# Optimization experiments

Hardware: AMD Instinct MI355X
Metric: run time of the kernel (lower is better)

The kernel has to match this reference:

```python
import jax, jax.numpy as jnp
import numpy as np

B, R, N, K, E = 128, 500, 500, 10, 128
H1 = 5 * E  # UnvisitedMLP hidden = embedding_dim * 5


def setup_inputs() -> dict:
    key = jax.random.key(0)
    ks = jax.random.split(key, 8)
    current = jax.random.randint(ks[0], (B, R), 0, N)
    distance = jax.random.uniform(ks[1], (B, N, N), dtype=jnp.float32)
    # unvisited cities, exercising the padding-index path in search_unvisited.
    visited = jax.random.uniform(ks[2], (B, R, N)) < 0.97
    masked = jnp.where(visited, -jnp.inf, 0.0).astype(jnp.float32)
    encoded_nodes = jax.random.normal(ks[3], (B, N, E), dtype=jnp.float32)
    w1 = jax.random.normal(ks[4], (H1, K * E), dtype=jnp.float32) * (1.0 / np.sqrt(K * E))
    b1 = jnp.zeros((H1,), dtype=jnp.float32)
    w2 = jax.random.normal(ks[5], (E, H1), dtype=jnp.float32) * (1.0 / np.sqrt(H1))
    b2 = jnp.zeros((E,), dtype=jnp.float32)
    return {"current": current, "distance": distance, "masked": masked,
            "encoded_nodes": encoded_nodes, "w1": w1, "b1": b1, "w2": w2, "b2": b2}


def _search_unvisited(current, distance, masked, k_near):
    # distance_filtered[b, r, :] = distance[b, current[b, r], :]  -> [B, R, N]
    b_idx = jnp.arange(current.shape[0])[:, None]
    distance_filtered = distance[b_idx, current, :]
    mask_unvisited = masked != -jnp.inf
    distance_masked = jnp.where(mask_unvisited, distance_filtered, jnp.inf)
    # k smallest == top-k of negated distances
    neg_vals, k_idx = jax.lax.top_k(-distance_masked, k_near)  # [B, R, K]
    is_inf = neg_vals == -jnp.inf  # entries that were +inf (no unvisited left)
    n_cities = distance.shape[1]
    return jnp.where(is_inf, n_cities, k_idx)  # padding index = problem_size


def _gather_pad0(encoded_nodes, idx):
    # pad encoded_nodes with a zero row at index N, then gather  -> [B, R, K, E]
    padded = jnp.concatenate(
        [encoded_nodes, jnp.zeros_like(encoded_nodes[:, :1, :])], axis=1)
    b_idx = jnp.arange(encoded_nodes.shape[0])[:, None, None]
    return padded[b_idx, idx, :]


def _pad_avg(a):
    # replace all-zero (padding) rows along K with the mean of non-zero rows
    is_zero = a.sum(axis=-1) == 0  # [B, R, K]
    nz_count = jnp.clip((~is_zero).sum(axis=-1).astype(jnp.float32), 1e-9)
    mean_vec = a.sum(axis=2) / nz_count[..., None]  # [B, R, E]
    return jnp.where(is_zero[..., None], mean_vec[:, :, None, :], a)


def reference(current, distance, masked, encoded_nodes, w1, b1, w2, b2):
    k_near = K
    idx = _search_unvisited(current, distance, masked, k_near)  # [B, R, K]
    emb = _gather_pad0(encoded_nodes, idx)                      # [B, R, K, E]
    emb = _pad_avg(emb)
    h = emb.reshape(emb.shape[0], emb.shape[1], k_near * emb.shape[-1])  # [B, R, K*E]
    h = jax.nn.relu(jnp.einsum('brf,hf->brh', h, w1) + b1)
    out = jnp.einsum('brh,eh->bre', h, w2) + b2  # [B, R, E]
    return out
```

## Files before the change

kernel.cpp:

```cpp
#include <hip/hip_runtime.h>
#include <cstdint>
#include <cstddef>

#define Bn   128
#define Rn   500
#define Nn   500
#define Kn   10
#define En   128
#define H1n  640
#define KEn  1280
#define Mn   (Bn * Rn)

typedef short s16x8 __attribute__((ext_vector_type(8)));
typedef float f32x4 __attribute__((ext_vector_type(4)));

__device__ __forceinline__ unsigned short f2bf(float x) {
    union { float f; unsigned int u; } v; v.f = x;
    unsigned int r = v.u + 0x7fffu + ((v.u >> 16) & 1u);
    return (unsigned short)(r >> 16);
}
__device__ __forceinline__ float bf2f(unsigned short u) {
    union { unsigned int u; float f; } v; v.u = ((unsigned int)u) << 16;
    return v.f;
}
__device__ __forceinline__ void gl2lds16(const void* g, void* l) {
    __builtin_amdgcn_global_load_lds(
        (const __attribute__((address_space(1))) unsigned int*)g,
        (__attribute__((address_space(3))) unsigned int*)l, 16, 0, 0);
}
__device__ __forceinline__ void drain_all() {
    asm volatile("s_waitcnt vmcnt(0) lgkmcnt(0)" ::: "memory");
}

__global__ void convw_kernel(const float* __restrict__ enc, const float* __restrict__ w1,
                             const float* __restrict__ w2,
                             unsigned short* __restrict__ encb, unsigned short* __restrict__ w1b,
                             unsigned short* __restrict__ w2b) {
    int i = blockIdx.x * 256 + threadIdx.x;
    if (i < (Bn * Nn * En) / 4) {
        float4 v = ((const float4*)enc)[i];
        ushort4 o; o.x = f2bf(v.x); o.y = f2bf(v.y); o.z = f2bf(v.z); o.w = f2bf(v.w);
        ((ushort4*)encb)[i] = o;
    }
    if (i < (H1n * KEn) / 4) {
        float4 v = ((const float4*)w1)[i];
        ushort4 o; o.x = f2bf(v.x); o.y = f2bf(v.y); o.z = f2bf(v.z); o.w = f2bf(v.w);
        ((ushort4*)w1b)[i] = o;
    }
    if (i < (En * H1n) / 4) {
        float4 v = ((const float4*)w2)[i];
        ushort4 o; o.x = f2bf(v.x); o.y = f2bf(v.y); o.z = f2bf(v.z); o.w = f2bf(v.w);
        ((ushort4*)w2b)[i] = o;
    }
}

__global__ __launch_bounds__(256) void select_kernel(const int* __restrict__ current,
                            const float* __restrict__ distance,
                            const float* __restrict__ masked,
                            const unsigned short* __restrict__ encb,
                            int* __restrict__ idx_out,
                            unsigned short* __restrict__ meanbb) {
    const int row  = blockIdx.x * 4 + (threadIdx.x >> 6);
    const int lane = threadIdx.x & 63;
    const int b    = row / Rn;
    const int cur  = current[row];
    const unsigned int* drow = (const unsigned int*)(distance + ((size_t)b * Nn + cur) * Nn);
    const unsigned int* mrow = (const unsigned int*)(masked + (size_t)row * Nn);

    unsigned long long key[8];
#pragma unroll
    for (int i = 0; i < 8; ++i) {
        int nn = lane + 64 * i;
        unsigned int fb = 0x7F800000u;
        if (nn < Nn) {
            unsigned int m = mrow[nn];
            unsigned int d = drow[nn];
            fb = (m == 0xFF800000u) ? 0x7F800000u : d;
        }
        key[i] = ((unsigned long long)fb << 32) | (unsigned int)nn;
    }

    int ids[Kn];
    int myid = Nn;
#pragma unroll
    for (int it = 0; it < Kn; ++it) {
        unsigned long long bk = key[0];
#pragma unroll
        for (int i = 1; i < 8; ++i) bk = (key[i] < bk) ? key[i] : bk;
#pragma unroll
        for (int off = 1; off < 64; off <<= 1) {
            unsigned long long ok = __shfl_xor(bk, off);
            bk = (ok < bk) ? ok : bk;
        }
        const int wid = ((bk >> 32) == 0x7F800000u) ? Nn : (int)(bk & 0xffffffffu);
        ids[it] = wid;
        if (lane == it) myid = wid;
#pragma unroll
        for (int i = 0; i < 8; ++i)
            if (key[i] == bk) key[i] = 0x7F800000FFFFFFFFull;
    }
    if (lane < Kn) idx_out[row * Kn + lane] = myid;

    const unsigned int* encu = (const unsigned int*)(encb + (size_t)b * Nn * En);
    float s0 = 0.f, s1 = 0.f; int cnt = 0;
#pragma unroll
    for (int k = 0; k < Kn; ++k) {
        const int id = ids[k];
        if (id < Nn) {
            unsigned int u = encu[id * (En / 2) + lane];
            s0 += bf2f((unsigned short)(u & 0xffffu));
            s1 += bf2f((unsigned short)(u >> 16));
            cnt++;
        }
    }
    float m0 = 0.f, m1 = 0.f;
    if (cnt > 0) { m0 = s0 / (float)cnt; m1 = s1 / (float)cnt; }
    unsigned int packed = (unsigned int)f2bf(m0) | ((unsigned int)f2bf(m1) << 16);
    ((unsigned int*)meanbb)[(size_t)row * (En / 2) + lane] = packed;
}

__global__ __launch_bounds__(256, 4) void gemm1_kernel(
        const unsigned short* __restrict__ encb, const unsigned short* __restrict__ meanbb,
        const int* __restrict__ idxb, const unsigned short* __restrict__ w1b,
        const float* __restrict__ b1, unsigned short* __restrict__ hbuf) {
    __shared__ alignas(16) unsigned short As[2][128 * 32];
    __shared__ alignas(16) unsigned short Bs[2][128 * 32];
    __shared__ int idxs[128 * Kn];

    const int p = blockIdx.x;
    const int L = (p & 7) * 313 + (p >> 3);
    if (L >= (Mn / 128) * (H1n / 128)) return;
    const int row0 = (L / 5) * 128;
    const int h0   = (L % 5) * 128;

    const int t    = threadIdx.x;
    const int lane = t & 63;
    const int wave = t >> 6;
    const int ln15 = lane & 15;
    const int q4   = lane >> 4;
    const int wm   = wave & 1;
    const int wn   = wave >> 1;

    for (int i = t; i < 128 * Kn; i += 256) idxs[i] = idxb[row0 * Kn + i];

    const int rl   = lane >> 2;
    const int sc   = lane & 3;
    const int coff = (sc ^ (rl & 3)) * 8;

    int lrow[2];
    const unsigned short* encB[2];
    const unsigned short* meanR[2];
    const unsigned short* w1R[2];
#pragma unroll
    for (int s = 0; s < 2; ++s) {
        lrow[s] = wave * 32 + s * 16 + rl;
        const int gr = row0 + lrow[s];
        const int bb = gr / Rn;
        encB[s]  = encb + (size_t)bb * Nn * En;
        meanR[s] = meanbb + (size_t)gr * En + coff;
        w1R[s]   = w1b + (size_t)(h0 + lrow[s]) * KEn + coff;
    }

    f32x4 acc[4][4];
#pragma unroll
    for (int i = 0; i < 4; ++i)
#pragma unroll
        for (int j = 0; j < 4; ++j)
            acc[i][j] = (f32x4){0.f, 0.f, 0.f, 0.f};

    auto issue = [&](int itk, int pb) {
        const int j   = itk >> 2;
        const int e0  = (itk & 3) * 32;
        const int kk0 = itk * 32;
#pragma unroll
        for (int s = 0; s < 2; ++s) {
            const int id = idxs[lrow[s] * Kn + j];
            const unsigned short* srcA = (id < Nn)
                ? (encB[s] + (size_t)id * En + e0 + coff)
                : (meanR[s] + e0);
            gl2lds16(srcA, &As[pb][(wave * 32 + s * 16) * 32]);
            gl2lds16(w1R[s] + kk0, &Bs[pb][(wave * 32 + s * 16) * 32]);
        }
    };

    drain_all();
    __syncthreads();
    issue(0, 0);

    for (int itk = 0; itk < KEn / 32; ++itk) {
        const int cur = itk & 1;
        drain_all();
        __syncthreads();
        if (itk + 1 < KEn / 32) issue(itk + 1, cur ^ 1);
        s16x8 af[4], bf[4];
#pragma unroll
        for (int i = 0; i < 4; ++i) {
            const int r = wm * 64 + i * 16 + ln15;
            af[i] = *(const s16x8*)&As[cur][r * 32 + (q4 ^ (r & 3)) * 8];
        }
#pragma unroll
        for (int jj = 0; jj < 4; ++jj) {
            const int r = wn * 64 + jj * 16 + ln15;
            bf[jj] = *(const s16x8*)&Bs[cur][r * 32 + (q4 ^ (r & 3)) * 8];
        }
#pragma unroll
        for (int i = 0; i < 4; ++i)
#pragma unroll
            for (int jj = 0; jj < 4; ++jj)
                acc[i][jj] = __builtin_amdgcn_mfma_f32_16x16x32_bf16(af[i], bf[jj], acc[i][jj], 0, 0, 0);
    }

#pragma unroll
    for (int i = 0; i < 4; ++i) {
#pragma unroll
        for (int jj = 0; jj < 4; ++jj) {
            const int h = h0 + wn * 64 + jj * 16 + ln15;
            const float bias = b1[h];
#pragma unroll
            for (int rg = 0; rg < 4; ++rg) {
                const int m = wm * 64 + i * 16 + q4 * 4 + rg;
                float vv = acc[i][jj][rg] + bias;
                vv = fmaxf(vv, 0.f);
                hbuf[(size_t)(row0 + m) * H1n + h] = f2bf(vv);
            }
        }
    }
}

__global__ __launch_bounds__(256, 4) void gemm2_kernel(
        const unsigned short* __restrict__ hbuf, const unsigned short* __restrict__ w2b,
        const float* __restrict__ b2, float* __restrict__ out) {
    __shared__ alignas(16) unsigned short As[2][128 * 32];
    __shared__ alignas(16) unsigned short Bs[2][128 * 32];

    const int row0 = blockIdx.x * 128;
    const int t    = threadIdx.x;
    const int lane = t & 63;
    const int wave = t >> 6;
    const int ln15 = lane & 15;
    const int q4   = lane >> 4;
    const int wm   = wave & 1;
    const int wn   = wave >> 1;

    const int rl   = lane >> 2;
    const int sc   = lane & 3;
    const int coff = (sc ^ (rl & 3)) * 8;

    const unsigned short* hrow[2];
    const unsigned short* w2row[2];
#pragma unroll
    for (int s = 0; s < 2; ++s) {
        const int lr = wave * 32 + s * 16 + rl;
        hrow[s]  = hbuf + (size_t)(row0 + lr) * H1n + coff;
        w2row[s] = w2b + (size_t)lr * H1n + coff;
    }

    f32x4 acc[4][4];
#pragma unroll
    for (int i = 0; i < 4; ++i)
#pragma unroll
        for (int j = 0; j < 4; ++j)
            acc[i][j] = (f32x4){0.f, 0.f, 0.f, 0.f};

    auto issue = [&](int itk, int pb) {
        const int kk0 = itk * 32;
#pragma unroll
        for (int s = 0; s < 2; ++s) {
            gl2lds16(hrow[s] + kk0, &As[pb][(wave * 32 + s * 16) * 32]);
            gl2lds16(w2row[s] + kk0, &Bs[pb][(wave * 32 + s * 16) * 32]);
        }
    };

    issue(0, 0);

    for (int itk = 0; itk < H1n / 32; ++itk) {
        const int cur = itk & 1;
        drain_all();
        __syncthreads();
        if (itk + 1 < H1n / 32) issue(itk + 1, cur ^ 1);
        s16x8 af[4], bf[4];
#pragma unroll
        for (int i = 0; i < 4; ++i) {
            const int r = wm * 64 + i * 16 + ln15;
            af[i] = *(const s16x8*)&As[cur][r * 32 + (q4 ^ (r & 3)) * 8];
        }
#pragma unroll
        for (int jj = 0; jj < 4; ++jj) {
            const int r = wn * 64 + jj * 16 + ln15;
            bf[jj] = *(const s16x8*)&Bs[cur][r * 32 + (q4 ^ (r & 3)) * 8];
        }
#pragma unroll
        for (int i = 0; i < 4; ++i)
#pragma unroll
            for (int jj = 0; jj < 4; ++jj)
                acc[i][jj] = __builtin_amdgcn_mfma_f32_16x16x32_bf16(af[i], bf[jj], acc[i][jj], 0, 0, 0);
    }

#pragma unroll
    for (int i = 0; i < 4; ++i) {
#pragma unroll
        for (int jj = 0; jj < 4; ++jj) {
            const int e = wn * 64 + jj * 16 + ln15;
            const float bias = b2[e];
#pragma unroll
            for (int rg = 0; rg < 4; ++rg) {
                const int m = wm * 64 + i * 16 + q4 * 4 + rg;
                out[(size_t)(row0 + m) * En + e] = acc[i][jj][rg] + bias;
            }
        }
    }
}

extern "C" void kernel_launch(void* const* d_in, const int* in_sizes, int n_in,
                              void* d_out, int out_size, void* d_ws, size_t ws_size,
                              hipStream_t stream) {
    const int*   current  = (const int*)d_in[0];
    const float* distance = (const float*)d_in[1];
    const float* masked   = (const float*)d_in[2];
    const float* encoded  = (const float*)d_in[3];
    const float* w1       = (const float*)d_in[4];
    const float* b1       = (const float*)d_in[5];
    const float* w2       = (const float*)d_in[6];
    const float* b2       = (const float*)d_in[7];
    float* out = (float*)d_out;

    char* ws = (char*)d_ws;
    const size_t OFF_IDX  = 0;
    const size_t OFF_ENCB = 2560000;
    const size_t OFF_MEAN = OFF_ENCB + 16384000;
    const size_t OFF_W1B  = OFF_MEAN + 16384000;
    const size_t OFF_W2B  = OFF_W1B + 1638400;
    const size_t OFF_H    = OFF_W2B + 163840;
    int*            idxb   = (int*)(ws + OFF_IDX);
    unsigned short* encb   = (unsigned short*)(ws + OFF_ENCB);
    unsigned short* meanbb = (unsigned short*)(ws + OFF_MEAN);
    unsigned short* w1b    = (unsigned short*)(ws + OFF_W1B);
    unsigned short* w2b    = (unsigned short*)(ws + OFF_W2B);
    unsigned short* hbuf   = (unsigned short*)(ws + OFF_H);

    convw_kernel<<<(Bn * Nn * En / 4 + 255) / 256, 256, 0, stream>>>(encoded, w1, w2, encb, w1b, w2b);
    select_kernel<<<Mn / 4, 256, 0, stream>>>(current, distance, masked, encb, idxb, meanbb);
    gemm1_kernel<<<2504, 256, 0, stream>>>(encb, meanbb, idxb, w1b, b1, hbuf);
    gemm2_kernel<<<Mn / 128, 256, 0, stream>>>(hbuf, w2b, b2, out);
}
```

Before: 484.1 us.

## Triple-buffer GEMM LDS tiles with partial vmcnt waits and new swizzle

Both GEMM kernels move from double-buffered to triple-buffered LDS tiles. Each iteration now waits with vmcnt(4) and a raw s_barrier instead of draining every outstanding load, so loads two tiles ahead stay in flight during compute. The LDS XOR swizzle changes from row&3 to (row>>1)&3 to reduce bank conflicts on the 16-byte fragment reads. LDS per block grows by half and launch bounds drop to 3 blocks per CU, which lowers occupancy. Correctness depends on the raw barrier and the lgkm ordering still being enough without an explicit lgkmcnt wait.

```diff
diff --git a/kernel.cpp b/kernel.cpp
--- a/kernel.cpp
+++ b/kernel.cpp
@@ -28,9 +28,9 @@
         (const __attribute__((address_space(1))) unsigned int*)g,
         (__attribute__((address_space(3))) unsigned int*)l, 16, 0, 0);
 }
-__device__ __forceinline__ void drain_all() {
-    asm volatile("s_waitcnt vmcnt(0) lgkmcnt(0)" ::: "memory");
-}
+__device__ __forceinline__ void wait_vm4() { asm volatile("s_waitcnt vmcnt(4)" ::: "memory"); }
+__device__ __forceinline__ void wait_vm0() { asm volatile("s_waitcnt vmcnt(0)" ::: "memory"); }
+__device__ __forceinline__ void barrier_raw() { asm volatile("s_barrier" ::: "memory"); }
 
 __global__ void convw_kernel(const float* __restrict__ enc, const float* __restrict__ w1,
                              const float* __restrict__ w2,
@@ -119,12 +119,12 @@
     ((unsigned int*)meanbb)[(size_t)row * (En / 2) + lane] = packed;
 }
 
-__global__ __launch_bounds__(256, 4) void gemm1_kernel(
+__global__ __launch_bounds__(256, 3) void gemm1_kernel(
         const unsigned short* __restrict__ encb, const unsigned short* __restrict__ meanbb,
         const int* __restrict__ idxb, const unsigned short* __restrict__ w1b,
         const float* __restrict__ b1, unsigned short* __restrict__ hbuf) {
-    __shared__ alignas(16) unsigned short As[2][128 * 32];
-    __shared__ alignas(16) unsigned short Bs[2][128 * 32];
+    __shared__ alignas(16) unsigned short As[3][128 * 32];
+    __shared__ alignas(16) unsigned short Bs[3][128 * 32];
     __shared__ int idxs[128 * Kn];
 
     const int p = blockIdx.x;
@@ -145,7 +145,7 @@
 
     const int rl   = lane >> 2;
     const int sc   = lane & 3;
-    const int coff = (sc ^ (rl & 3)) * 8;
+    const int coff = (sc ^ ((rl >> 1) & 3)) * 8;
 
     int lrow[2];
     const unsigned short* encB[2];
@@ -183,31 +183,37 @@
         }
     };
 
-    drain_all();
     __syncthreads();
     issue(0, 0);
-
-    for (int itk = 0; itk < KEn / 32; ++itk) {
-        const int cur = itk & 1;
-        drain_all();
-        __syncthreads();
-        if (itk + 1 < KEn / 32) issue(itk + 1, cur ^ 1);
+    issue(1, 1);
+
+    const int NT = KEn / 32;
+    const int sw = ((ln15 >> 1) & 3);
+    int cb = 0;
+    for (int itk = 0; itk < NT; ++itk) {
+        if (itk < NT - 1) wait_vm4(); else wait_vm0();
+        barrier_raw();
+        if (itk + 2 < NT) {
+            int pb = cb + 2; if (pb >= 3) pb -= 3;
+            issue(itk + 2, pb);
+        }
         s16x8 af[4], bf[4];
 #pragma unroll
         for (int i = 0; i < 4; ++i) {
             const int r = wm * 64 + i * 16 + ln15;
-            af[i] = *(const s16x8*)&As[cur][r * 32 + (q4 ^ (r & 3)) * 8];
+            af[i] = *(const s16x8*)&As[cb][r * 32 + (q4 ^ sw) * 8];
         }
 #pragma unroll
         for (int jj = 0; jj < 4; ++jj) {
             const int r = wn * 64 + jj * 16 + ln15;
-            bf[jj] = *(const s16x8*)&Bs[cur][r * 32 + (q4 ^ (r & 3)) * 8];
+            bf[jj] = *(const s16x8*)&Bs[cb][r * 32 + (q4 ^ sw) * 8];
         }
 #pragma unroll
         for (int i = 0; i < 4; ++i)
 #pragma unroll
             for (int jj = 0; jj < 4; ++jj)
                 acc[i][jj] = __builtin_amdgcn_mfma_f32_16x16x32_bf16(af[i], bf[jj], acc[i][jj], 0, 0, 0);
+        cb = (cb == 2) ? 0 : cb + 1;
     }
 
 #pragma unroll
@@ -227,11 +233,11 @@
     }
 }
 
-__global__ __launch_bounds__(256, 4) void gemm2_kernel(
+__global__ __launch_bounds__(256, 3) void gemm2_kernel(
         const unsigned short* __restrict__ hbuf, const unsigned short* __restrict__ w2b,
         const float* __restrict__ b2, float* __restrict__ out) {
-    __shared__ alignas(16) unsigned short As[2][128 * 32];
-    __shared__ alignas(16) unsigned short Bs[2][128 * 32];
+    __shared__ alignas(16) unsigned short As[3][128 * 32];
+    __shared__ alignas(16) unsigned short Bs[3][128 * 32];
 
     const int row0 = blockIdx.x * 128;
     const int t    = threadIdx.x;
@@ -244,7 +250,7 @@
 
     const int rl   = lane >> 2;
     const int sc   = lane & 3;
-    const int coff = (sc ^ (rl & 3)) * 8;
+    const int coff = (sc ^ ((rl >> 1) & 3)) * 8;
 
     const unsigned short* hrow[2];
     const unsigned short* w2row[2];
@@ -272,28 +278,35 @@
     };
 
     issue(0, 0);
-
-    for (int itk = 0; itk < H1n / 32; ++itk) {
-        const int cur = itk & 1;
-        drain_all();
-        __syncthreads();
-        if (itk + 1 < H1n / 32) issue(itk + 1, cur ^ 1);
+    issue(1, 1);
+
+    const int NT = H1n / 32;
+    const int sw = ((ln15 >> 1) & 3);
+    int cb = 0;
+    for (int itk = 0; itk < NT; ++itk) {
+        if (itk < NT - 1) wait_vm4(); else wait_vm0();
+        barrier_raw();
+        if (itk + 2 < NT) {
+            int pb = cb + 2; if (pb >= 3) pb -= 3;
+            issue(itk + 2, pb);
+        }
         s16x8 af[4], bf[4];
 #pragma unroll
         for (int i = 0; i < 4; ++i) {
             const int r = wm * 64 + i * 16 + ln15;
-            af[i] = *(const s16x8*)&As[cur][r * 32 + (q4 ^ (r & 3)) * 8];
+            af[i] = *(const s16x8*)&As[cb][r * 32 + (q4 ^ sw) * 8];
         }
 #pragma unroll
         for (int jj = 0; jj < 4; ++jj) {
             const int r = wn * 64 + jj * 16 + ln15;
-            bf[jj] = *(const s16x8*)&Bs[cur][r * 32 + (q4 ^ (r & 3)) * 8];
+            bf[jj] = *(const s16x8*)&Bs[cb][r * 32 + (q4 ^ sw) * 8];
         }
 #pragma unroll
         for (int i = 0; i < 4; ++i)
 #pragma unroll
             for (int jj = 0; jj < 4; ++jj)
                 acc[i][jj] = __builtin_amdgcn_mfma_f32_16x16x32_bf16(af[i], bf[jj], acc[i][jj], 0, 0, 0);
+        cb = (cb == 2) ? 0 : cb + 1;
     }
 
 #pragma unroll
```

New measurement: 509.3 us. 5.2% more time.
